# Kernel optimization log

Measured on AMD Instinct MI355X. Metric: run time of the kernel, lower is better.

Reference implementation:

```python
import jax, jax.numpy as jnp
import numpy as np


def _pairwise_sq_dist_mean(x):
    """Mean over feature dim of pairwise squared distances: D[i,j] = mean_k (x[j,k]-x[i,k])^2.
    Uses the ||a||^2 + ||b||^2 - 2ab identity instead of the O(n^2*d) broadcast."""
    d = x.shape[1]
    sq = jnp.sum(x * x, axis=1)  # [n]
    gram = x @ x.T               # [n, n]
    return (sq[:, None] + sq[None, :] - 2.0 * gram) / d


def setup_inputs() -> dict:
    key = jax.random.key(0)
    k1, k2 = jax.random.split(key)
    noises = jax.random.normal(k1, (4096, 256), dtype=jnp.float32)
    images = jax.random.normal(k2, (4096, 3, 64, 64), dtype=jnp.float32)
    return {"noises": noises, "images": images}


def reference(noises, images):
    if images.ndim > 2:
        images = images.reshape(images.shape[0], -1)
    images_dist = _pairwise_sq_dist_mean(images)  # [B, B]
    noises_dist = _pairwise_sq_dist_mean(noises)  # [B, B]
    return jnp.exp(jnp.mean(-images_dist * noises_dist))
```

## Files before the change

kernel.cpp:

```cpp
#include <hip/hip_runtime.h>
#include <stdint.h>
#include <math.h>

typedef __attribute__((ext_vector_type(8))) short short8;
typedef __attribute__((ext_vector_type(4))) float f32x4;

typedef __attribute__((address_space(1))) const uint32_t g_u32;
typedef __attribute__((address_space(3))) uint32_t l_u32;

static __device__ __forceinline__ uint16_t f2bf(float f) {
  union { float f; uint32_t u; } v; v.f = f;
  uint32_t r = (v.u + 0x7FFFu + ((v.u >> 16) & 1u)) >> 16;
  return (uint16_t)r;
}

static __device__ __forceinline__ float bf2f(uint16_t u) {
  union { uint32_t u; float f; } v; v.u = ((uint32_t)u) << 16;
  return v.f;
}

static __device__ __forceinline__ float waveReduceSum(float x) {
#pragma unroll
  for (int m = 32; m > 0; m >>= 1) x += __shfl_xor(x, m, 64);
  return x;
}

__global__ __launch_bounds__(256) void k_zero(float* __restrict__ p, int n4) {
  const int i = blockIdx.x * 256 + threadIdx.x;
  if (i < n4) reinterpret_cast<float4*>(p)[i] = float4{0.f, 0.f, 0.f, 0.f};
}

__global__ __launch_bounds__(256) void k_nt(const float* __restrict__ N,
                                            uint16_t* __restrict__ Nt,
                                            float* __restrict__ b,
                                            float* __restrict__ sn) {
  __shared__ __align__(16) uint16_t T[256 * 72];
  const int i0 = blockIdx.x * 64;
  const int tid = threadIdx.x;
  const int wave = tid >> 6, lane = tid & 63;
  float sq[16];
  float snacc0 = 0.f, snacc1 = 0.f, snacc2 = 0.f, snacc3 = 0.f;
#pragma unroll
  for (int it = 0; it < 16; ++it) {
    const int k = wave + it * 4;
    const int l4 = lane * 4;
    const float4 v = *reinterpret_cast<const float4*>(N + (size_t)(i0 + k) * 256 + l4);
    T[(l4 + 0) * 72 + k] = f2bf(v.x);
    T[(l4 + 1) * 72 + k] = f2bf(v.y);
    T[(l4 + 2) * 72 + k] = f2bf(v.z);
    T[(l4 + 3) * 72 + k] = f2bf(v.w);
    sq[it] = v.x * v.x + v.y * v.y + v.z * v.z + v.w * v.w;
    snacc0 += v.x; snacc1 += v.y; snacc2 += v.z; snacc3 += v.w;
  }
#pragma unroll
  for (int m = 1; m < 64; m <<= 1) {
#pragma unroll
    for (int it = 0; it < 16; ++it) sq[it] += __shfl_xor(sq[it], m, 64);
  }
  float myv = sq[0];
#pragma unroll
  for (int it = 1; it < 16; ++it) myv = (lane == it) ? sq[it] : myv;
  if (lane < 16) b[i0 + wave + lane * 4] = myv;
  {
    const int l4 = lane * 4;
    atomicAdd(&sn[l4 + 0], snacc0); atomicAdd(&sn[l4 + 1], snacc1);
    atomicAdd(&sn[l4 + 2], snacc2); atomicAdd(&sn[l4 + 3], snacc3);
  }
  __syncthreads();
  const int l = tid;
#pragma unroll
  for (int tt = 0; tt < 2; ++tt) {
    const int tg = blockIdx.x * 2 + tt;
#pragma unroll
    for (int c = 0; c < 4; ++c) {
      const short8 v = *reinterpret_cast<const short8*>(&T[l * 72 + tt * 32 + c * 8]);
      *reinterpret_cast<short8*>((char*)Nt + (size_t)tg * 16384 + l * 64 +
                                 ((c ^ (l & 3)) << 4)) = v;
    }
  }
}

__global__ __launch_bounds__(256) void k_h1(const float* __restrict__ N,
                                            const float* __restrict__ sn,
                                            float* __restrict__ h1) {
  const int wave = threadIdx.x >> 6, lane = threadIdx.x & 63;
  const int i = blockIdx.x * 4 + wave;
  const float4 v = *reinterpret_cast<const float4*>(N + (size_t)i * 256 + lane * 4);
  const float4 s = *reinterpret_cast<const float4*>(sn + lane * 4);
  float d = v.x * s.x + v.y * s.y + v.z * s.z + v.w * s.w;
  d = waveReduceSum(d);
  if (lane == 0) h1[i] = d;
}

__global__ __launch_bounds__(256, 3) void k_gemm_f3(const float* __restrict__ X,
                                                    const uint16_t* __restrict__ Nt,
                                                    uint16_t* __restrict__ Mb,
                                                    const float* __restrict__ bvec,
                                                    const float* __restrict__ h1v,
                                                    float* __restrict__ sx,
                                                    float* __restrict__ cx,
                                                    float* __restrict__ scal,
                                                    int B, int D1) {
  __shared__ __align__(16) uint16_t NB[2][8192];
  __shared__ __align__(16) uint16_t AB[2][64 * 40];
  __shared__ float SR[3][4];
  const int tid = threadIdx.x;
  const int w = tid >> 6, lane = tid & 63;
  const int lr = lane & 15, lh = lane >> 4;
  const int nks = B >> 7;
  const int pt = blockIdx.x >> 2, kc = blockIdx.x & 3;
  const int pbase = pt << 6;
  const int ks0 = kc * nks;

  f32x4 acc[4][4];
#pragma unroll
  for (int i = 0; i < 4; ++i)
#pragma unroll
    for (int j = 0; j < 4; ++j) acc[i][j] = (f32x4){0.f, 0.f, 0.f, 0.f};

  const int ap = tid & 63, ak8 = (tid >> 6) << 3;
  const float* Xbase = X + (size_t)(ks0 * 32 + ak8) * D1 + pbase + ap;
  float xr[8];
  float4 bv0, bv1, hv0, hv1;
  float s1 = 0.f, sb = 0.f, sh = 0.f, sxa = 0.f, cxa = 0.f;

#define GLL_B(S, BUF)                                                              \
  {                                                                                \
    const char* gsrc_ = (const char*)Nt + (size_t)(ks0 + (S)) * 16384 +            \
                        ((size_t)w << 10) + (size_t)lane * 16;                     \
    _Pragma("unroll")                                                              \
    for (int j_ = 0; j_ < 4; ++j_) {                                               \
      __builtin_amdgcn_global_load_lds((g_u32*)(gsrc_ + ((size_t)j_ << 12)),       \
                                       (l_u32*)&NB[BUF][(j_ * 4 + w) << 9],        \
                                       16, 0, 0);                                  \
    }                                                                              \
  }
#define A_LOADS(S)                                                                 \
  {                                                                                \
    const float* p_ = Xbase + (size_t)(S) * 32 * D1;                               \
    _Pragma("unroll")                                                              \
    for (int r_ = 0; r_ < 8; ++r_) xr[r_] = p_[(size_t)r_ * D1];                   \
    const int ib_ = ks0 * 32 + (S) * 32 + ak8;                                     \
    bv0 = *reinterpret_cast<const float4*>(bvec + ib_);                            \
    bv1 = *reinterpret_cast<const float4*>(bvec + ib_ + 4);                        \
    hv0 = *reinterpret_cast<const float4*>(h1v + ib_);                             \
    hv1 = *reinterpret_cast<const float4*>(h1v + ib_ + 4);                         \
  }

  GLL_B(0, 0);
  A_LOADS(0);

  for (int s = 0; s < nks; ++s) {
    const int buf = s & 1;
    {
      union { uint16_t u[8]; short8 v; } pk;
      const float bb[8] = {bv0.x, bv0.y, bv0.z, bv0.w, bv1.x, bv1.y, bv1.z, bv1.w};
      const float hh[8] = {hv0.x, hv0.y, hv0.z, hv0.w, hv1.x, hv1.y, hv1.z, hv1.w};
#pragma unroll
      for (int r = 0; r < 8; ++r) {
        const float x = xr[r];
        pk.u[r] = f2bf(x);
        const float x2 = x * x;
        s1 += x2;
        sb += bb[r] * x2;
        sh += hh[r] * x2;
        sxa += x;
        cxa += bb[r] * x;
      }
      *reinterpret_cast<short8*>(&AB[buf][ap * 40 + ak8]) = pk.v;
    }
    __syncthreads();
    if (s + 1 < nks) {
      GLL_B(s + 1, buf ^ 1);
      A_LOADS(s + 1);
    }
    short8 af[4], bfv[4];
#pragma unroll
    for (int ps = 0; ps < 4; ++ps)
      af[ps] = *reinterpret_cast<const short8*>(&AB[buf][(ps * 16 + lr) * 40 + lh * 8]);
#pragma unroll
    for (int q = 0; q < 4; ++q) {
      const int l = (w << 6) + (q << 4) + lr;
      bfv[q] = *reinterpret_cast<const short8*>(&NB[buf][l * 32 + ((lh ^ (l & 3)) << 3)]);
    }
#pragma unroll
    for (int ps = 0; ps < 4; ++ps)
#pragma unroll
      for (int q = 0; q < 4; ++q)
        acc[ps][q] = __builtin_amdgcn_mfma_f32_16x16x32_bf16(af[ps], bfv[q], acc[ps][q], 0, 0, 0);
    __syncthreads();
  }
#undef GLL_B
#undef A_LOADS

  uint16_t* Mk = Mb + (size_t)kc * ((size_t)D1 * 256);
#pragma unroll
  for (int ps = 0; ps < 4; ++ps)
#pragma unroll
    for (int q = 0; q < 4; ++q) {
      const int l = (w << 6) + (q << 4) + lr;
      const int p0 = pbase + ps * 16 + lh * 4;
      ushort4 st;
      st.x = f2bf(acc[ps][q][0]); st.y = f2bf(acc[ps][q][1]);
      st.z = f2bf(acc[ps][q][2]); st.w = f2bf(acc[ps][q][3]);
      *reinterpret_cast<ushort4*>(&Mk[(size_t)l * D1 + p0]) = st;
    }

  atomicAdd(&sx[pbase + ap], sxa);
  atomicAdd(&cx[pbase + ap], cxa);

  s1 = waveReduceSum(s1); sb = waveReduceSum(sb); sh = waveReduceSum(sh);
  if (lane == 0) { SR[0][w] = s1; SR[1][w] = sb; SR[2][w] = sh; }
  __syncthreads();
  if (tid == 0) {
    atomicAdd(&scal[0], SR[0][0] + SR[0][1] + SR[0][2] + SR[0][3]);
    atomicAdd(&scal[1], SR[1][0] + SR[1][1] + SR[1][2] + SR[1][3]);
    atomicAdd(&scal[2], SR[2][0] + SR[2][1] + SR[2][2] + SR[2][3]);
  }
}

__global__ __launch_bounds__(256) void k_square(const uint16_t* __restrict__ Mb,
                                                float* __restrict__ Fp,
                                                int n8, int slice) {
  __shared__ float red[4];
  float s = 0.f;
  for (int idx = blockIdx.x * 256 + threadIdx.x; idx < n8; idx += gridDim.x * 256) {
    union { short8 v; uint16_t u[8]; } m0, m1, m2, m3;
    m0.v = *reinterpret_cast<const short8*>(Mb + (size_t)idx * 8);
    m1.v = *reinterpret_cast<const short8*>(Mb + (size_t)idx * 8 + (size_t)slice);
    m2.v = *reinterpret_cast<const short8*>(Mb + (size_t)idx * 8 + 2 * (size_t)slice);
    m3.v = *reinterpret_cast<const short8*>(Mb + (size_t)idx * 8 + 3 * (size_t)slice);
#pragma unroll
    for (int e = 0; e < 8; ++e) {
      const float v = bf2f(m0.u[e]) + bf2f(m1.u[e]) + bf2f(m2.u[e]) + bf2f(m3.u[e]);
      s += v * v;
    }
  }
  s = waveReduceSum(s);
  const int wave = threadIdx.x >> 6, lane = threadIdx.x & 63;
  if (lane == 0) red[wave] = s;
  __syncthreads();
  if (threadIdx.x == 0) atomicAdd(Fp, red[0] + red[1] + red[2] + red[3]);
}

__global__ __launch_bounds__(256) void k_final3(const float* __restrict__ scal,
                                                const float* __restrict__ b,
                                                const float* __restrict__ sx,
                                                const float* __restrict__ cx,
                                                float* __restrict__ out,
                                                int B, int D1) {
  const int tid = threadIdx.x;
  float sb_ = 0.f, t2_ = 0.f;
  for (int i = tid; i < B; i += 256) sb_ += b[i];
  for (int k = tid; k < D1; k += 256) t2_ += sx[k] * cx[k];
  sb_ = waveReduceSum(sb_); t2_ = waveReduceSum(t2_);
  __shared__ float R[2][4];
  const int wave = tid >> 6, lane = tid & 63;
  if (lane == 0) { R[0][wave] = sb_; R[1][wave] = t2_; }
  __syncthreads();
  if (tid == 0) {
    double Sb = 0, T2 = 0;
    for (int w = 0; w < 4; ++w) { Sb += R[0][w]; T2 += R[1][w]; }
    const double Sa = scal[0], Sab = scal[1], T1 = scal[2], F = scal[3];
    const double total = 2.0 * (double)B * Sab + 2.0 * Sa * Sb - 4.0 * T1 - 4.0 * T2 + 4.0 * F;
    const double denom = (double)D1 * 256.0 * (double)B * (double)B;
    out[0] = (float)exp(-total / denom);
  }
}

__global__ __launch_bounds__(256) void k_noise_b(const float* __restrict__ N,
                                                 float* __restrict__ b) {
  const int wave = threadIdx.x >> 6, lane = threadIdx.x & 63;
  const int i = blockIdx.x * 4 + wave;
  const float4 v = *reinterpret_cast<const float4*>(N + (size_t)i * 256 + lane * 4);
  float s = v.x * v.x + v.y * v.y + v.z * v.z + v.w * v.w;
  s = waveReduceSum(s);
  if (lane == 0) b[i] = s;
}

__global__ __launch_bounds__(256) void k_x_pass(const float* __restrict__ X,
                                                const float* __restrict__ b,
                                                float* __restrict__ a,
                                                float* __restrict__ sx,
                                                float* __restrict__ cx, int D1) {
  const int ncb = D1 >> 10;
  const int colblk = blockIdx.x % ncb;
  const int rowblk = blockIdx.x / ncb;
  const int wv = threadIdx.x >> 6, lane = threadIdx.x & 63;
  const int col = (colblk << 10) + (wv << 8) + (lane << 2);
  const int row0 = rowblk << 6;
  float s0 = 0.f, s1 = 0.f, s2 = 0.f, s3 = 0.f;
  float c0 = 0.f, c1 = 0.f, c2 = 0.f, c3 = 0.f;
  const float* p = X + (size_t)row0 * D1 + col;
  for (int r8 = 0; r8 < 64; r8 += 8) {
    float asq[8];
#pragma unroll
    for (int r = 0; r < 8; ++r) {
      const float4 v = *reinterpret_cast<const float4*>(p + (size_t)(r8 + r) * D1);
      const float bi = b[row0 + r8 + r];
      s0 += v.x; s1 += v.y; s2 += v.z; s3 += v.w;
      c0 += bi * v.x; c1 += bi * v.y; c2 += bi * v.z; c3 += bi * v.w;
      asq[r] = v.x * v.x + v.y * v.y + v.z * v.z + v.w * v.w;
    }
#pragma unroll
    for (int m = 1; m < 64; m <<= 1) {
#pragma unroll
      for (int r = 0; r < 8; ++r) asq[r] += __shfl_xor(asq[r], m, 64);
    }
    float myv = asq[0];
#pragma unroll
    for (int r = 1; r < 8; ++r) myv = (lane == r) ? asq[r] : myv;
    if (lane < 8) atomicAdd(&a[row0 + r8 + lane], myv);
  }
  atomicAdd(&sx[col + 0], s0); atomicAdd(&sx[col + 1], s1);
  atomicAdd(&sx[col + 2], s2); atomicAdd(&sx[col + 3], s3);
  atomicAdd(&cx[col + 0], c0); atomicAdd(&cx[col + 1], c1);
  atomicAdd(&cx[col + 2], c2); atomicAdd(&cx[col + 3], c3);
}

__global__ __launch_bounds__(256) void k_noise2(const float* __restrict__ N,
                                                const float* __restrict__ a,
                                                float* __restrict__ sn,
                                                float* __restrict__ an) {
  const int t = threadIdx.x;
  const int i0 = blockIdx.x << 6;
  float ssn = 0.f, san = 0.f;
  for (int r = 0; r < 64; ++r) {
    const int i = i0 + r;
    const float v = N[(size_t)i * 256 + t];
    ssn += v;
    san += a[i] * v;
  }
  atomicAdd(&sn[t], ssn);
  atomicAdd(&an[t], san);
}

__global__ __launch_bounds__(256) void k_gemm_f(const float* __restrict__ X,
                                                const float* __restrict__ Nz,
                                                float* __restrict__ Fout,
                                                int B, int D1) {
  __shared__ uint16_t Abf[64 * 40];
  __shared__ uint16_t Bbf[256 * 40];
  __shared__ float red[4];
  const int tid = threadIdx.x;
  const int pbase = blockIdx.x << 6;
  const int wave = tid >> 6, lane = tid & 63;
  const int lr = lane & 15, lh = lane >> 4;

  f32x4 acc[4][4];
#pragma unroll
  for (int i = 0; i < 4; ++i)
#pragma unroll
    for (int j = 0; j < 4; ++j) acc[i][j] = (f32x4){0.f, 0.f, 0.f, 0.f};

  const int igx = tid & 7, p4x = ((tid >> 3) & 15) << 2;
  const int ign0 = tid & 7, l4n0 = (tid >> 3) << 2;
  const int ign1 = (tid + 256) & 7, l4n1 = ((tid + 256) >> 3) << 2;

  float4 xr0, xr1, xr2, xr3;
  float4 n0r0, n0r1, n0r2, n0r3;
  float4 n1r0, n1r1, n1r2, n1r3;

  auto load_stage = [&](int i0) {
    if (tid < 128) {
      const float* src = X + (size_t)(i0 + igx * 4) * D1 + pbase + p4x;
      xr0 = *reinterpret_cast<const float4*>(src);
      xr1 = *reinterpret_cast<const float4*>(src + D1);
      xr2 = *reinterpret_cast<const float4*>(src + 2 * (size_t)D1);
      xr3 = *reinterpret_cast<const float4*>(src + 3 * (size_t)D1);
    }
    {
      const float* src = Nz + (size_t)(i0 + ign0 * 4) * 256 + l4n0;
      n0r0 = *reinterpret_cast<const float4*>(src);
      n0r1 = *reinterpret_cast<const float4*>(src + 256);
      n0r2 = *reinterpret_cast<const float4*>(src + 512);
      n0r3 = *reinterpret_cast<const float4*>(src + 768);
    }
    {
      const float* src = Nz + (size_t)(i0 + ign1 * 4) * 256 + l4n1;
      n1r0 = *reinterpret_cast<const float4*>(src);
      n1r1 = *reinterpret_cast<const float4*>(src + 256);
      n1r2 = *reinterpret_cast<const float4*>(src + 512);
      n1r3 = *reinterpret_cast<const float4*>(src + 768);
    }
  };

  auto store_stage = [&]() {
    ushort4 w;
    if (tid < 128) {
      w.x = f2bf(xr0.x); w.y = f2bf(xr1.x); w.z = f2bf(xr2.x); w.w = f2bf(xr3.x);
      *reinterpret_cast<ushort4*>(&Abf[(p4x + 0) * 40 + igx * 4]) = w;
      w.x = f2bf(xr0.y); w.y = f2bf(xr1.y); w.z = f2bf(xr2.y); w.w = f2bf(xr3.y);
      *reinterpret_cast<ushort4*>(&Abf[(p4x + 1) * 40 + igx * 4]) = w;
      w.x = f2bf(xr0.z); w.y = f2bf(xr1.z); w.z = f2bf(xr2.z); w.w = f2bf(xr3.z);
      *reinterpret_cast<ushort4*>(&Abf[(p4x + 2) * 40 + igx * 4]) = w;
      w.x = f2bf(xr0.w); w.y = f2bf(xr1.w); w.z = f2bf(xr2.w); w.w = f2bf(xr3.w);
      *reinterpret_cast<ushort4*>(&Abf[(p4x + 3) * 40 + igx * 4]) = w;
    }
    w.x = f2bf(n0r0.x); w.y = f2bf(n0r1.x); w.z = f2bf(n0r2.x); w.w = f2bf(n0r3.x);
    *reinterpret_cast<ushort4*>(&Bbf[(l4n0 + 0) * 40 + ign0 * 4]) = w;
    w.x = f2bf(n0r0.y); w.y = f2bf(n0r1.y); w.z = f2bf(n0r2.y); w.w = f2bf(n0r3.y);
    *reinterpret_cast<ushort4*>(&Bbf[(l4n0 + 1) * 40 + ign0 * 4]) = w;
    w.x = f2bf(n0r0.z); w.y = f2bf(n0r1.z); w.z = f2bf(n0r2.z); w.w = f2bf(n0r3.z);
    *reinterpret_cast<ushort4*>(&Bbf[(l4n0 + 2) * 40 + ign0 * 4]) = w;
    w.x = f2bf(n0r0.w); w.y = f2bf(n0r1.w); w.z = f2bf(n0r2.w); w.w = f2bf(n0r3.w);
    *reinterpret_cast<ushort4*>(&Bbf[(l4n0 + 3) * 40 + ign0 * 4]) = w;

    w.x = f2bf(n1r0.x); w.y = f2bf(n1r1.x); w.z = f2bf(n1r2.x); w.w = f2bf(n1r3.x);
    *reinterpret_cast<ushort4*>(&Bbf[(l4n1 + 0) * 40 + ign1 * 4]) = w;
    w.x = f2bf(n1r0.y); w.y = f2bf(n1r1.y); w.z = f2bf(n1r2.y); w.w = f2bf(n1r3.y);
    *reinterpret_cast<ushort4*>(&Bbf[(l4n1 + 1) * 40 + ign1 * 4]) = w;
    w.x = f2bf(n1r0.z); w.y = f2bf(n1r1.z); w.z = f2bf(n1r2.z); w.w = f2bf(n1r3.z);
    *reinterpret_cast<ushort4*>(&Bbf[(l4n1 + 2) * 40 + ign1 * 4]) = w;
    w.x = f2bf(n1r0.w); w.y = f2bf(n1r1.w); w.z = f2bf(n1r2.w); w.w = f2bf(n1r3.w);
    *reinterpret_cast<ushort4*>(&Bbf[(l4n1 + 3) * 40 + ign1 * 4]) = w;
  };

  load_stage(0);
  for (int i0 = 0; i0 < B; i0 += 32) {
    store_stage();
    __syncthreads();
    if (i0 + 32 < B) load_stage(i0 + 32);

    short8 af[4], bfv[4];
#pragma unroll
    for (int ps = 0; ps < 4; ++ps)
      af[ps] = *reinterpret_cast<const short8*>(&Abf[(ps * 16 + lr) * 40 + lh * 8]);
#pragma unroll
    for (int q = 0; q < 4; ++q)
      bfv[q] = *reinterpret_cast<const short8*>(&Bbf[((wave * 4 + q) * 16 + lr) * 40 + lh * 8]);
#pragma unroll
    for (int ps = 0; ps < 4; ++ps)
#pragma unroll
      for (int q = 0; q < 4; ++q)
        acc[ps][q] = __builtin_amdgcn_mfma_f32_16x16x32_bf16(af[ps], bfv[q], acc[ps][q], 0, 0, 0);
    __syncthreads();
  }

  float loc = 0.f;
#pragma unroll
  for (int ps = 0; ps < 4; ++ps)
#pragma unroll
    for (int q = 0; q < 4; ++q)
#pragma unroll
      for (int e = 0; e < 4; ++e) loc += acc[ps][q][e] * acc[ps][q][e];
  loc = waveReduceSum(loc);
  if (lane == 0) red[wave] = loc;
  __syncthreads();
  if (tid == 0) atomicAdd(Fout, red[0] + red[1] + red[2] + red[3]);
}

__global__ __launch_bounds__(256) void k_final(const float* __restrict__ a,
                                               const float* __restrict__ b,
                                               const float* __restrict__ sx,
                                               const float* __restrict__ cx,
                                               const float* __restrict__ sn,
                                               const float* __restrict__ an,
                                               const float* __restrict__ Fp,
                                               float* __restrict__ out, int B, int D1) {
  const int tid = threadIdx.x;
  float sa = 0.f, sb = 0.f, sab = 0.f, t2 = 0.f;
  for (int i = tid; i < B; i += 256) {
    const float ai = a[i], bi = b[i];
    sa += ai; sb += bi; sab += ai * bi;
  }
  float t1 = an[tid] * sn[tid];
  for (int k = tid; k < D1; k += 256) t2 += cx[k] * sx[k];

  sa = waveReduceSum(sa); sb = waveReduceSum(sb); sab = waveReduceSum(sab);
  t1 = waveReduceSum(t1); t2 = waveReduceSum(t2);
  __shared__ float R[5][4];
  const int wave = tid >> 6, lane = tid & 63;
  if (lane == 0) { R[0][wave] = sa; R[1][wave] = sb; R[2][wave] = sab; R[3][wave] = t1; R[4][wave] = t2; }
  __syncthreads();
  if (tid == 0) {
    double Sa = 0, Sb = 0, Sab = 0, T1 = 0, T2 = 0;
    for (int w = 0; w < 4; ++w) {
      Sa += R[0][w]; Sb += R[1][w]; Sab += R[2][w]; T1 += R[3][w]; T2 += R[4][w];
    }
    const double F = (double)Fp[0];
    const double total = 2.0 * (double)B * Sab + 2.0 * Sa * Sb - 4.0 * T1 - 4.0 * T2 + 4.0 * F;
    const double denom = (double)D1 * 256.0 * (double)B * (double)B;
    out[0] = (float)exp(-total / denom);
  }
}

extern "C" void kernel_launch(void* const* d_in, const int* in_sizes, int n_in,
                              void* d_out, int out_size, void* d_ws, size_t ws_size,
                              hipStream_t stream) {
  const float* noises = (const float*)d_in[0];
  const float* images = (const float*)d_in[1];
  const int B = in_sizes[0] / 256;
  const int D1 = in_sizes[1] / B;
  float* outf = (float*)d_out;
  float* ws = (float*)d_ws;

  float* sx   = ws;
  float* cx   = ws + D1;
  float* sn   = ws + 2 * D1;
  float* scal = ws + 2 * D1 + 256;
  float* b    = ws + 2 * D1 + 272;
  float* h1   = b + B;
  const size_t nt_off_f = (size_t)2 * D1 + 272 + 2 * (size_t)B;
  const size_t nt_off_a = (nt_off_f + 3) & ~(size_t)3;
  uint16_t* Nt = (uint16_t*)(ws + nt_off_a);
  const size_t mb_off_f = nt_off_a + ((size_t)B * 256) / 2;
  uint16_t* Mb = (uint16_t*)(ws + mb_off_f);
  const size_t need = (mb_off_f + 2 * (size_t)D1 * 256) * sizeof(float);

  if (ws_size >= need) {
    const int nzero4 = (2 * D1 + 272) / 4;
    k_zero<<<(nzero4 + 255) / 256, 256, 0, stream>>>(ws, nzero4);
    k_nt<<<B / 64, 256, 0, stream>>>(noises, Nt, b, sn);
    k_h1<<<B / 4, 256, 0, stream>>>(noises, sn, h1);
    k_gemm_f3<<<(D1 / 64) * 4, 256, 0, stream>>>(images, Nt, Mb, b, h1, sx, cx, scal, B, D1);
    k_square<<<512, 256, 0, stream>>>(Mb, &scal[3], D1 * 256 / 8, D1 * 256);
    k_final3<<<1, 256, 0, stream>>>(scal, b, sx, cx, outf, B, D1);
  } else {
    float* a2  = ws;
    float* b2  = ws + B;
    float* sx2 = ws + 2 * B;
    float* cx2 = ws + 2 * B + D1;
    float* sn2 = ws + 2 * B + 2 * D1;
    float* an2 = ws + 2 * B + 2 * D1 + 256;
    float* Fp2 = ws + 2 * B + 2 * D1 + 512;
    const int nzero4 = (2 * B + 2 * D1 + 516) / 4;
    k_zero<<<(nzero4 + 255) / 256, 256, 0, stream>>>(ws, nzero4);
    k_noise_b<<<B / 4, 256, 0, stream>>>(noises, b2);
    k_x_pass<<<(D1 / 1024) * (B / 64), 256, 0, stream>>>(images, b2, a2, sx2, cx2, D1);
    k_noise2<<<B / 64, 256, 0, stream>>>(noises, a2, sn2, an2);
    k_gemm_f<<<D1 / 64, 256, 0, stream>>>(images, noises, Fp2, B, D1);
    k_final<<<1, 256, 0, stream>>>(a2, b2, sx2, cx2, sn2, an2, Fp2, outf, B, D1);
  }
}
```

Before: 151.5 us.

## Split image transpose/bf16 packing into separate pass feeding a pure-MFMA GEMM

```diff
diff --git a/kernel.cpp b/kernel.cpp
--- a/kernel.cpp
+++ b/kernel.cpp
@@ -90,6 +90,211 @@
   float d = v.x * s.x + v.y * s.y + v.z * s.z + v.w * s.w;
   d = waveReduceSum(d);
   if (lane == 0) h1[i] = d;
+}
+
+__global__ __launch_bounds__(256) void k_xt(const float* __restrict__ X,
+                                            const float* __restrict__ b,
+                                            const float* __restrict__ h1,
+                                            uint16_t* __restrict__ Xt,
+                                            float* __restrict__ sx,
+                                            float* __restrict__ cx,
+                                            float* __restrict__ scalA,
+                                            int B, int D1) {
+  __shared__ float T[64 * 65];
+  __shared__ float colS[64], colC[64];
+  __shared__ float SR[3][4];
+  const int tid = threadIdx.x;
+  const int npt = D1 >> 6;
+  const int pt = blockIdx.x % npt;
+  const int ti = blockIdx.x / npt;
+  const int i0 = ti << 6, p0 = pt << 6;
+  if (tid < 64) { colS[tid] = 0.f; colC[tid] = 0.f; }
+  __syncthreads();
+
+  const int r0 = tid >> 4;
+  const int c4 = (tid & 15) << 2;
+  float s1 = 0.f, sb = 0.f, sh = 0.f;
+  float cs0 = 0.f, cs1 = 0.f, cs2 = 0.f, cs3 = 0.f;
+  float cc0 = 0.f, cc1 = 0.f, cc2 = 0.f, cc3 = 0.f;
+#pragma unroll
+  for (int rr = 0; rr < 4; ++rr) {
+    const int r = r0 + rr * 16;
+    const int i = i0 + r;
+    const float4 v = *reinterpret_cast<const float4*>(X + (size_t)i * D1 + p0 + c4);
+    const float bi = b[i], hi = h1[i];
+    const float d = v.x * v.x + v.y * v.y + v.z * v.z + v.w * v.w;
+    s1 += d; sb += bi * d; sh += hi * d;
+    cs0 += v.x; cs1 += v.y; cs2 += v.z; cs3 += v.w;
+    cc0 += bi * v.x; cc1 += bi * v.y; cc2 += bi * v.z; cc3 += bi * v.w;
+    *reinterpret_cast<float4*>(&T[r * 65 + c4]) = v;
+  }
+  atomicAdd(&colS[c4 + 0], cs0); atomicAdd(&colS[c4 + 1], cs1);
+  atomicAdd(&colS[c4 + 2], cs2); atomicAdd(&colS[c4 + 3], cs3);
+  atomicAdd(&colC[c4 + 0], cc0); atomicAdd(&colC[c4 + 1], cc1);
+  atomicAdd(&colC[c4 + 2], cc2); atomicAdd(&colC[c4 + 3], cc3);
+  __syncthreads();
+
+  const int pl = tid >> 2;
+  const int slot = tid & 3;
+  const int oct = slot ^ (pl & 3);
+  uint16_t* img = Xt + ((size_t)pt * (B >> 5) + (size_t)(ti << 1)) * 2048;
+  {
+    union { uint16_t u[8]; short8 v8; } pk;
+#pragma unroll
+    for (int j = 0; j < 8; ++j) pk.u[j] = f2bf(T[(oct * 8 + j) * 65 + pl]);
+    *reinterpret_cast<short8*>(img + tid * 8) = pk.v8;
+#pragma unroll
+    for (int j = 0; j < 8; ++j) pk.u[j] = f2bf(T[(32 + oct * 8 + j) * 65 + pl]);
+    *reinterpret_cast<short8*>(img + 2048 + tid * 8) = pk.v8;
+  }
+
+  s1 = waveReduceSum(s1); sb = waveReduceSum(sb); sh = waveReduceSum(sh);
+  const int wave = tid >> 6, lane = tid & 63;
+  if (lane == 0) { SR[0][wave] = s1; SR[1][wave] = sb; SR[2][wave] = sh; }
+  if (tid < 64) {
+    atomicAdd(&sx[p0 + tid], colS[tid]);
+    atomicAdd(&cx[p0 + tid], colC[tid]);
+  }
+  __syncthreads();
+  if (tid == 0) {
+    float* slotp = scalA + (size_t)(blockIdx.x & 63) * 4;
+    atomicAdd(&slotp[0], SR[0][0] + SR[0][1] + SR[0][2] + SR[0][3]);
+    atomicAdd(&slotp[1], SR[1][0] + SR[1][1] + SR[1][2] + SR[1][3]);
+    atomicAdd(&slotp[2], SR[2][0] + SR[2][1] + SR[2][2] + SR[2][3]);
+  }
+}
+
+__global__ __launch_bounds__(256, 3) void k_gemm_f4(const uint16_t* __restrict__ Xt,
+                                                    const uint16_t* __restrict__ Nt,
+                                                    uint16_t* __restrict__ Mb,
+                                                    int B, int D1) {
+  __shared__ __align__(16) uint16_t NB[2][8192];
+  __shared__ __align__(16) uint16_t AB[2][2048];
+  const int tid = threadIdx.x;
+  const int w = tid >> 6, lane = tid & 63;
+  const int lr = lane & 15, lh = lane >> 4;
+  const int nks = B >> 7;
+  const int tks = B >> 5;
+  const int pt = blockIdx.x >> 2, kc = blockIdx.x & 3;
+  const int pbase = pt << 6;
+  const int ks0 = kc * nks;
+
+  f32x4 acc[4][4];
+#pragma unroll
+  for (int i = 0; i < 4; ++i)
+#pragma unroll
+    for (int j = 0; j < 4; ++j) acc[i][j] = (f32x4){0.f, 0.f, 0.f, 0.f};
+
+#define GLL_AB(S, BUF)                                                             \
+  {                                                                                \
+    const char* bs_ = (const char*)Nt + (size_t)(ks0 + (S)) * 16384 +              \
+                      ((size_t)w << 10) + (size_t)lane * 16;                       \
+    _Pragma("unroll")                                                              \
+    for (int j_ = 0; j_ < 4; ++j_) {                                               \
+      __builtin_amdgcn_global_load_lds((g_u32*)(bs_ + ((size_t)j_ << 12)),         \
+                                       (l_u32*)&NB[BUF][(j_ * 4 + w) << 9],        \
+                                       16, 0, 0);                                  \
+    }                                                                              \
+    const char* as_ = (const char*)Xt + ((size_t)pt * tks + ks0 + (S)) * 4096 +    \
+                      ((size_t)w << 10) + (size_t)lane * 16;                       \
+    __builtin_amdgcn_global_load_lds((g_u32*)as_, (l_u32*)&AB[BUF][w << 9],        \
+                                     16, 0, 0);                                    \
+  }
+
+  GLL_AB(0, 0);
+  for (int s = 0; s < nks; ++s) {
+    const int buf = s & 1;
+    __syncthreads();
+    if (s + 1 < nks) GLL_AB(s + 1, buf ^ 1);
+    short8 af[4], bfv[4];
+#pragma unroll
+    for (int ps = 0; ps < 4; ++ps) {
+      const int p = ps * 16 + lr;
+      af[ps] = *reinterpret_cast<const short8*>(&AB[buf][p * 32 + ((lh ^ (p & 3)) << 3)]);
+    }
+#pragma unroll
+    for (int q = 0; q < 4; ++q) {
+      const int l = (w << 6) + (q << 4) + lr;
+      bfv[q] = *reinterpret_cast<const short8*>(&NB[buf][l * 32 + ((lh ^ (l & 3)) << 3)]);
+    }
+#pragma unroll
+    for (int ps = 0; ps < 4; ++ps)
+#pragma unroll
+      for (int q = 0; q < 4; ++q)
+        acc[ps][q] = __builtin_amdgcn_mfma_f32_16x16x32_bf16(af[ps], bfv[q], acc[ps][q], 0, 0, 0);
+  }
+#undef GLL_AB
+
+  uint16_t* Mk = Mb + (size_t)kc * ((size_t)D1 * 256);
+#pragma unroll
+  for (int ps = 0; ps < 4; ++ps)
+#pragma unroll
+    for (int q = 0; q < 4; ++q) {
+      const int l = (w << 6) + (q << 4) + lr;
+      const int p0e = pbase + ps * 16 + lh * 4;
+      ushort4 st;
+      st.x = f2bf(acc[ps][q][0]); st.y = f2bf(acc[ps][q][1]);
+      st.z = f2bf(acc[ps][q][2]); st.w = f2bf(acc[ps][q][3]);
+      *reinterpret_cast<ushort4*>(&Mk[(size_t)l * D1 + p0e]) = st;
+    }
+}
+
+__global__ __launch_bounds__(256) void k_square(const uint16_t* __restrict__ Mb,
+                                                float* __restrict__ Fp,
+                                                int n8, int slice) {
+  __shared__ float red[4];
+  float s = 0.f;
+  for (int idx = blockIdx.x * 256 + threadIdx.x; idx < n8; idx += gridDim.x * 256) {
+    union { short8 v; uint16_t u[8]; } m0, m1, m2, m3;
+    m0.v = *reinterpret_cast<const short8*>(Mb + (size_t)idx * 8);
+    m1.v = *reinterpret_cast<const short8*>(Mb + (size_t)idx * 8 + (size_t)slice);
+    m2.v = *reinterpret_cast<const short8*>(Mb + (size_t)idx * 8 + 2 * (size_t)slice);
+    m3.v = *reinterpret_cast<const short8*>(Mb + (size_t)idx * 8 + 3 * (size_t)slice);
+#pragma unroll
+    for (int e = 0; e < 8; ++e) {
+      const float v = bf2f(m0.u[e]) + bf2f(m1.u[e]) + bf2f(m2.u[e]) + bf2f(m3.u[e]);
+      s += v * v;
+    }
+  }
+  s = waveReduceSum(s);
+  const int wave = threadIdx.x >> 6, lane = threadIdx.x & 63;
+  if (lane == 0) red[wave] = s;
+  __syncthreads();
+  if (threadIdx.x == 0) atomicAdd(Fp, red[0] + red[1] + red[2] + red[3]);
+}
+
+__global__ __launch_bounds__(256) void k_final4(const float* __restrict__ scalA,
+                                                const float* __restrict__ Fp,
+                                                const float* __restrict__ b,
+                                                const float* __restrict__ sx,
+                                                const float* __restrict__ cx,
+                                                float* __restrict__ out,
+                                                int B, int D1) {
+  const int tid = threadIdx.x;
+  float sa_ = 0.f, sab_ = 0.f, t1_ = 0.f, sb_ = 0.f, t2_ = 0.f;
+  if (tid < 64) {
+    sa_ = scalA[tid * 4 + 0];
+    sab_ = scalA[tid * 4 + 1];
+    t1_ = scalA[tid * 4 + 2];
+  }
+  for (int i = tid; i < B; i += 256) sb_ += b[i];
+  for (int k = tid; k < D1; k += 256) t2_ += sx[k] * cx[k];
+  sa_ = waveReduceSum(sa_); sab_ = waveReduceSum(sab_); t1_ = waveReduceSum(t1_);
+  sb_ = waveReduceSum(sb_); t2_ = waveReduceSum(t2_);
+  __shared__ float R[5][4];
+  const int wave = tid >> 6, lane = tid & 63;
+  if (lane == 0) { R[0][wave] = sa_; R[1][wave] = sab_; R[2][wave] = t1_; R[3][wave] = sb_; R[4][wave] = t2_; }
+  __syncthreads();
+  if (tid == 0) {
+    double Sa = 0, Sab = 0, T1 = 0, Sb = 0, T2 = 0;
+    for (int w = 0; w < 4; ++w) {
+      Sa += R[0][w]; Sab += R[1][w]; T1 += R[2][w]; Sb += R[3][w]; T2 += R[4][w];
+    }
+    const double F = (double)Fp[0];
+    const double total = 2.0 * (double)B * Sab + 2.0 * Sa * Sb - 4.0 * T1 - 4.0 * T2 + 4.0 * F;
+    const double denom = (double)D1 * 256.0 * (double)B * (double)B;
+    out[0] = (float)exp(-total / denom);
+  }
 }
 
 __global__ __launch_bounds__(256, 3) void k_gemm_f3(const float* __restrict__ X,
@@ -161,11 +366,8 @@
         const float x = xr[r];
         pk.u[r] = f2bf(x);
         const float x2 = x * x;
-        s1 += x2;
-        sb += bb[r] * x2;
-        sh += hh[r] * x2;
-        sxa += x;
-        cxa += bb[r] * x;
+        s1 += x2; sb += bb[r] * x2; sh += hh[r] * x2;
+        sxa += x; cxa += bb[r] * x;
       }
       *reinterpret_cast<short8*>(&AB[buf][ap * 40 + ak8]) = pk.v;
     }
@@ -217,30 +419,6 @@
     atomicAdd(&scal[1], SR[1][0] + SR[1][1] + SR[1][2] + SR[1][3]);
     atomicAdd(&scal[2], SR[2][0] + SR[2][1] + SR[2][2] + SR[2][3]);
   }
-}
-
-__global__ __launch_bounds__(256) void k_square(const uint16_t* __restrict__ Mb,
-                                                float* __restrict__ Fp,
-                                                int n8, int slice) {
-  __shared__ float red[4];
-  float s = 0.f;
-  for (int idx = blockIdx.x * 256 + threadIdx.x; idx < n8; idx += gridDim.x * 256) {
-    union { short8 v; uint16_t u[8]; } m0, m1, m2, m3;
-    m0.v = *reinterpret_cast<const short8*>(Mb + (size_t)idx * 8);
-    m1.v = *reinterpret_cast<const short8*>(Mb + (size_t)idx * 8 + (size_t)slice);
-    m2.v = *reinterpret_cast<const short8*>(Mb + (size_t)idx * 8 + 2 * (size_t)slice);
-    m3.v = *reinterpret_cast<const short8*>(Mb + (size_t)idx * 8 + 3 * (size_t)slice);
-#pragma unroll
-    for (int e = 0; e < 8; ++e) {
-      const float v = bf2f(m0.u[e]) + bf2f(m1.u[e]) + bf2f(m2.u[e]) + bf2f(m3.u[e]);
-      s += v * v;
-    }
-  }
-  s = waveReduceSum(s);
-  const int wave = threadIdx.x >> 6, lane = threadIdx.x & 63;
-  if (lane == 0) red[wave] = s;
-  __syncthreads();
-  if (threadIdx.x == 0) atomicAdd(Fp, red[0] + red[1] + red[2] + red[3]);
 }
 
 __global__ __launch_bounds__(256) void k_final3(const float* __restrict__ scal,
@@ -268,223 +446,6 @@
   }
 }
 
-__global__ __launch_bounds__(256) void k_noise_b(const float* __restrict__ N,
-                                                 float* __restrict__ b) {
-  const int wave = threadIdx.x >> 6, lane = threadIdx.x & 63;
-  const int i = blockIdx.x * 4 + wave;
-  const float4 v = *reinterpret_cast<const float4*>(N + (size_t)i * 256 + lane * 4);
-  float s = v.x * v.x + v.y * v.y + v.z * v.z + v.w * v.w;
-  s = waveReduceSum(s);
-  if (lane == 0) b[i] = s;
-}
-
-__global__ __launch_bounds__(256) void k_x_pass(const float* __restrict__ X,
-                                                const float* __restrict__ b,
-                                                float* __restrict__ a,
-                                                float* __restrict__ sx,
-                                                float* __restrict__ cx, int D1) {
-  const int ncb = D1 >> 10;
-  const int colblk = blockIdx.x % ncb;
-  const int rowblk = blockIdx.x / ncb;
-  const int wv = threadIdx.x >> 6, lane = threadIdx.x & 63;
-  const int col = (colblk << 10) + (wv << 8) + (lane << 2);
-  const int row0 = rowblk << 6;
-  float s0 = 0.f, s1 = 0.f, s2 = 0.f, s3 = 0.f;
-  float c0 = 0.f, c1 = 0.f, c2 = 0.f, c3 = 0.f;
-  const float* p = X + (size_t)row0 * D1 + col;
-  for (int r8 = 0; r8 < 64; r8 += 8) {
-    float asq[8];
-#pragma unroll
-    for (int r = 0; r < 8; ++r) {
-      const float4 v = *reinterpret_cast<const float4*>(p + (size_t)(r8 + r) * D1);
-      const float bi = b[row0 + r8 + r];
-      s0 += v.x; s1 += v.y; s2 += v.z; s3 += v.w;
-      c0 += bi * v.x; c1 += bi * v.y; c2 += bi * v.z; c3 += bi * v.w;
-      asq[r] = v.x * v.x + v.y * v.y + v.z * v.z + v.w * v.w;
-    }
-#pragma unroll
-    for (int m = 1; m < 64; m <<= 1) {
-#pragma unroll
-      for (int r = 0; r < 8; ++r) asq[r] += __shfl_xor(asq[r], m, 64);
-    }
-    float myv = asq[0];
-#pragma unroll
-    for (int r = 1; r < 8; ++r) myv = (lane == r) ? asq[r] : myv;
-    if (lane < 8) atomicAdd(&a[row0 + r8 + lane], myv);
-  }
-  atomicAdd(&sx[col + 0], s0); atomicAdd(&sx[col + 1], s1);
-  atomicAdd(&sx[col + 2], s2); atomicAdd(&sx[col + 3], s3);
-  atomicAdd(&cx[col + 0], c0); atomicAdd(&cx[col + 1], c1);
-  atomicAdd(&cx[col + 2], c2); atomicAdd(&cx[col + 3], c3);
-}
-
-__global__ __launch_bounds__(256) void k_noise2(const float* __restrict__ N,
-                                                const float* __restrict__ a,
-                                                float* __restrict__ sn,
-                                                float* __restrict__ an) {
-  const int t = threadIdx.x;
-  const int i0 = blockIdx.x << 6;
-  float ssn = 0.f, san = 0.f;
-  for (int r = 0; r < 64; ++r) {
-    const int i = i0 + r;
-    const float v = N[(size_t)i * 256 + t];
-    ssn += v;
-    san += a[i] * v;
-  }
-  atomicAdd(&sn[t], ssn);
-  atomicAdd(&an[t], san);
-}
-
-__global__ __launch_bounds__(256) void k_gemm_f(const float* __restrict__ X,
-                                                const float* __restrict__ Nz,
-                                                float* __restrict__ Fout,
-                                                int B, int D1) {
-  __shared__ uint16_t Abf[64 * 40];
-  __shared__ uint16_t Bbf[256 * 40];
-  __shared__ float red[4];
-  const int tid = threadIdx.x;
-  const int pbase = blockIdx.x << 6;
-  const int wave = tid >> 6, lane = tid & 63;
-  const int lr = lane & 15, lh = lane >> 4;
-
-  f32x4 acc[4][4];
-#pragma unroll
-  for (int i = 0; i < 4; ++i)
-#pragma unroll
-    for (int j = 0; j < 4; ++j) acc[i][j] = (f32x4){0.f, 0.f, 0.f, 0.f};
-
-  const int igx = tid & 7, p4x = ((tid >> 3) & 15) << 2;
-  const int ign0 = tid & 7, l4n0 = (tid >> 3) << 2;
-  const int ign1 = (tid + 256) & 7, l4n1 = ((tid + 256) >> 3) << 2;
-
-  float4 xr0, xr1, xr2, xr3;
-  float4 n0r0, n0r1, n0r2, n0r3;
-  float4 n1r0, n1r1, n1r2, n1r3;
-
-  auto load_stage = [&](int i0) {
-    if (tid < 128) {
-      const float* src = X + (size_t)(i0 + igx * 4) * D1 + pbase + p4x;
-      xr0 = *reinterpret_cast<const float4*>(src);
-      xr1 = *reinterpret_cast<const float4*>(src + D1);
-      xr2 = *reinterpret_cast<const float4*>(src + 2 * (size_t)D1);
-      xr3 = *reinterpret_cast<const float4*>(src + 3 * (size_t)D1);
-    }
-    {
-      const float* src = Nz + (size_t)(i0 + ign0 * 4) * 256 + l4n0;
-      n0r0 = *reinterpret_cast<const float4*>(src);
-      n0r1 = *reinterpret_cast<const float4*>(src + 256);
-      n0r2 = *reinterpret_cast<const float4*>(src + 512);
-      n0r3 = *reinterpret_cast<const float4*>(src + 768);
-    }
-    {
-      const float* src = Nz + (size_t)(i0 + ign1 * 4) * 256 + l4n1;
-      n1r0 = *reinterpret_cast<const float4*>(src);
-      n1r1 = *reinterpret_cast<const float4*>(src + 256);
-      n1r2 = *reinterpret_cast<const float4*>(src + 512);
-      n1r3 = *reinterpret_cast<const float4*>(src + 768);
-    }
-  };
-
-  auto store_stage = [&]() {
-    ushort4 w;
-    if (tid < 128) {
-      w.x = f2bf(xr0.x); w.y = f2bf(xr1.x); w.z = f2bf(xr2.x); w.w = f2bf(xr3.x);
-      *reinterpret_cast<ushort4*>(&Abf[(p4x + 0) * 40 + igx * 4]) = w;
-      w.x = f2bf(xr0.y); w.y = f2bf(xr1.y); w.z = f2bf(xr2.y); w.w = f2bf(xr3.y);
-      *reinterpret_cast<ushort4*>(&Abf[(p4x + 1) * 40 + igx * 4]) = w;
-      w.x = f2bf(xr0.z); w.y = f2bf(xr1.z); w.z = f2bf(xr2.z); w.w = f2bf(xr3.z);
-      *reinterpret_cast<ushort4*>(&Abf[(p4x + 2) * 40 + igx * 4]) = w;
-      w.x = f2bf(xr0.w); w.y = f2bf(xr1.w); w.z = f2bf(xr2.w); w.w = f2bf(xr3.w);
-      *reinterpret_cast<ushort4*>(&Abf[(p4x + 3) * 40 + igx * 4]) = w;
-    }
-    w.x = f2bf(n0r0.x); w.y = f2bf(n0r1.x); w.z = f2bf(n0r2.x); w.w = f2bf(n0r3.x);
-    *reinterpret_cast<ushort4*>(&Bbf[(l4n0 + 0) * 40 + ign0 * 4]) = w;
-    w.x = f2bf(n0r0.y); w.y = f2bf(n0r1.y); w.z = f2bf(n0r2.y); w.w = f2bf(n0r3.y);
-    *reinterpret_cast<ushort4*>(&Bbf[(l4n0 + 1) * 40 + ign0 * 4]) = w;
-    w.x = f2bf(n0r0.z); w.y = f2bf(n0r1.z); w.z = f2bf(n0r2.z); w.w = f2bf(n0r3.z);
-    *reinterpret_cast<ushort4*>(&Bbf[(l4n0 + 2) * 40 + ign0 * 4]) = w;
-    w.x = f2bf(n0r0.w); w.y = f2bf(n0r1.w); w.z = f2bf(n0r2.w); w.w = f2bf(n0r3.w);
-    *reinterpret_cast<ushort4*>(&Bbf[(l4n0 + 3) * 40 + ign0 * 4]) = w;
-
-    w.x = f2bf(n1r0.x); w.y = f2bf(n1r1.x); w.z = f2bf(n1r2.x); w.w = f2bf(n1r3.x);
-    *reinterpret_cast<ushort4*>(&Bbf[(l4n1 + 0) * 40 + ign1 * 4]) = w;
-    w.x = f2bf(n1r0.y); w.y = f2bf(n1r1.y); w.z = f2bf(n1r2.y); w.w = f2bf(n1r3.y);
-    *reinterpret_cast<ushort4*>(&Bbf[(l4n1 + 1) * 40 + ign1 * 4]) = w;
-    w.x = f2bf(n1r0.z); w.y = f2bf(n1r1.z); w.z = f2bf(n1r2.z); w.w = f2bf(n1r3.z);
-    *reinterpret_cast<ushort4*>(&Bbf[(l4n1 + 2) * 40 + ign1 * 4]) = w;
-    w.x = f2bf(n1r0.w); w.y = f2bf(n1r1.w); w.z = f2bf(n1r2.w); w.w = f2bf(n1r3.w);
-    *reinterpret_cast<ushort4*>(&Bbf[(l4n1 + 3) * 40 + ign1 * 4]) = w;
-  };
-
-  load_stage(0);
-  for (int i0 = 0; i0 < B; i0 += 32) {
-    store_stage();
-    __syncthreads();
-    if (i0 + 32 < B) load_stage(i0 + 32);
-
-    short8 af[4], bfv[4];
-#pragma unroll
-    for (int ps = 0; ps < 4; ++ps)
-      af[ps] = *reinterpret_cast<const short8*>(&Abf[(ps * 16 + lr) * 40 + lh * 8]);
-#pragma unroll
-    for (int q = 0; q < 4; ++q)
-      bfv[q] = *reinterpret_cast<const short8*>(&Bbf[((wave * 4 + q) * 16 + lr) * 40 + lh * 8]);
-#pragma unroll
-    for (int ps = 0; ps < 4; ++ps)
-#pragma unroll
-      for (int q = 0; q < 4; ++q)
-        acc[ps][q] = __builtin_amdgcn_mfma_f32_16x16x32_bf16(af[ps], bfv[q], acc[ps][q], 0, 0, 0);
-    __syncthreads();
-  }
-
-  float loc = 0.f;
-#pragma unroll
-  for (int ps = 0; ps < 4; ++ps)
-#pragma unroll
-    for (int q = 0; q < 4; ++q)
-#pragma unroll
-      for (int e = 0; e < 4; ++e) loc += acc[ps][q][e] * acc[ps][q][e];
-  loc = waveReduceSum(loc);
-  if (lane == 0) red[wave] = loc;
-  __syncthreads();
-  if (tid == 0) atomicAdd(Fout, red[0] + red[1] + red[2] + red[3]);
-}
-
-__global__ __launch_bounds__(256) void k_final(const float* __restrict__ a,
-                                               const float* __restrict__ b,
-                                               const float* __restrict__ sx,
-                                               const float* __restrict__ cx,
-                                               const float* __restrict__ sn,
-                                               const float* __restrict__ an,
-                                               const float* __restrict__ Fp,
-                                               float* __restrict__ out, int B, int D1) {
-  const int tid = threadIdx.x;
-  float sa = 0.f, sb = 0.f, sab = 0.f, t2 = 0.f;
-  for (int i = tid; i < B; i += 256) {
-    const float ai = a[i], bi = b[i];
-    sa += ai; sb += bi; sab += ai * bi;
-  }
-  float t1 = an[tid] * sn[tid];
-  for (int k = tid; k < D1; k += 256) t2 += cx[k] * sx[k];
-
-  sa = waveReduceSum(sa); sb = waveReduceSum(sb); sab = waveReduceSum(sab);
-  t1 = waveReduceSum(t1); t2 = waveReduceSum(t2);
-  __shared__ float R[5][4];
-  const int wave = tid >> 6, lane = tid & 63;
-  if (lane == 0) { R[0][wave] = sa; R[1][wave] = sb; R[2][wave] = sab; R[3][wave] = t1; R[4][wave] = t2; }
-  __syncthreads();
-  if (tid == 0) {
-    double Sa = 0, Sb = 0, Sab = 0, T1 = 0, T2 = 0;
-    for (int w = 0; w < 4; ++w) {
-      Sa += R[0][w]; Sb += R[1][w]; Sab += R[2][w]; T1 += R[3][w]; T2 += R[4][w];
-    }
-    const double F = (double)Fp[0];
-    const double total = 2.0 * (double)B * Sab + 2.0 * Sa * Sb - 4.0 * T1 - 4.0 * T2 + 4.0 * F;
-    const double denom = (double)D1 * 256.0 * (double)B * (double)B;
-    out[0] = (float)exp(-total / denom);
-  }
-}
-
 extern "C" void kernel_launch(void* const* d_in, const int* in_sizes, int n_in,
                               void* d_out, int out_size, void* d_ws, size_t ws_size,
                               hipStream_t stream) {
@@ -495,41 +456,48 @@
   float* outf = (float*)d_out;
   float* ws = (float*)d_ws;
 
-  float* sx   = ws;
-  float* cx   = ws + D1;
-  float* sn   = ws + 2 * D1;
-  float* scal = ws + 2 * D1 + 256;
-  float* b    = ws + 2 * D1 + 272;
-  float* h1   = b + B;
-  const size_t nt_off_f = (size_t)2 * D1 + 272 + 2 * (size_t)B;
-  const size_t nt_off_a = (nt_off_f + 3) & ~(size_t)3;
-  uint16_t* Nt = (uint16_t*)(ws + nt_off_a);
-  const size_t mb_off_f = nt_off_a + ((size_t)B * 256) / 2;
-  uint16_t* Mb = (uint16_t*)(ws + mb_off_f);
-  const size_t need = (mb_off_f + 2 * (size_t)D1 * 256) * sizeof(float);
-
-  if (ws_size >= need) {
-    const int nzero4 = (2 * D1 + 272) / 4;
+  float* sx    = ws;
+  float* cx    = ws + D1;
+  float* sn    = ws + 2 * D1;
+  float* scalA = ws + 2 * D1 + 256;
+  float* Fp    = ws + 2 * D1 + 512;
+  float* b     = ws + 2 * D1 + 544;
+  float* h1    = b + B;
+  const size_t nt_off = ((size_t)2 * D1 + 544 + 2 * (size_t)B + 3) & ~(size_t)3;
+  uint16_t* Nt = (uint16_t*)(ws + nt_off);
+  const size_t xt_off = nt_off + ((size_t)B * 256) / 2;
+  uint16_t* Xt = (uint16_t*)(ws + xt_off);
+  const size_t xt_floats = ((size_t)D1 / 64) * ((size_t)B / 32) * 1024;
+  const size_t mb_off = xt_off + xt_floats;
+  uint16_t* Mb = (uint16_t*)(ws + mb_off);
+  const size_t need1 = (mb_off + 2 * (size_t)D1 * 256) * sizeof(float);
+
+  if (ws_size >= need1) {
+    const int nzero4 = (2 * D1 + 544) / 4;
     k_zero<<<(nzero4 + 255) / 256, 256, 0, stream>>>(ws, nzero4);
     k_nt<<<B / 64, 256, 0, stream>>>(noises, Nt, b, sn);
     k_h1<<<B / 4, 256, 0, stream>>>(noises, sn, h1);
-    k_gemm_f3<<<(D1 / 64) * 4, 256, 0, stream>>>(images, Nt, Mb, b, h1, sx, cx, scal, B, D1);
-    k_square<<<512, 256, 0, stream>>>(Mb, &scal[3], D1 * 256 / 8, D1 * 256);
-    k_final3<<<1, 256, 0, stream>>>(scal, b, sx, cx, outf, B, D1);
+    k_xt<<<(B / 64) * (D1 / 64), 256, 0, stream>>>(images, b, h1, Xt, sx, cx, scalA, B, D1);
+    k_gemm_f4<<<(D1 / 64) * 4, 256, 0, stream>>>(Xt, Nt, Mb, B, D1);
+    k_square<<<512, 256, 0, stream>>>(Mb, Fp, D1 * 256 / 8, D1 * 256);
+    k_final4<<<1, 256, 0, stream>>>(scalA, Fp, b, sx, cx, outf, B, D1);
   } else {
-    float* a2  = ws;
-    float* b2  = ws + B;
-    float* sx2 = ws + 2 * B;
-    float* cx2 = ws + 2 * B + D1;
-    float* sn2 = ws + 2 * B + 2 * D1;
-    float* an2 = ws + 2 * B + 2 * D1 + 256;
-    float* Fp2 = ws + 2 * B + 2 * D1 + 512;
-    const int nzero4 = (2 * B + 2 * D1 + 516) / 4;
+    float* sx2   = ws;
+    float* cx2   = ws + D1;
+    float* sn2   = ws + 2 * D1;
+    float* scal2 = ws + 2 * D1 + 256;
+    float* b2    = ws + 2 * D1 + 272;
+    float* h12   = b2 + B;
+    const size_t nt2_off = ((size_t)2 * D1 + 272 + 2 * (size_t)B + 3) & ~(size_t)3;
+    uint16_t* Nt2 = (uint16_t*)(ws + nt2_off);
+    const size_t mb2_off = nt2_off + ((size_t)B * 256) / 2;
+    uint16_t* Mb2 = (uint16_t*)(ws + mb2_off);
+    const int nzero4 = (2 * D1 + 272) / 4;
     k_zero<<<(nzero4 + 255) / 256, 256, 0, stream>>>(ws, nzero4);
-    k_noise_b<<<B / 4, 256, 0, stream>>>(noises, b2);
-    k_x_pass<<<(D1 / 1024) * (B / 64), 256, 0, stream>>>(images, b2, a2, sx2, cx2, D1);
-    k_noise2<<<B / 64, 256, 0, stream>>>(noises, a2, sn2, an2);
-    k_gemm_f<<<D1 / 64, 256, 0, stream>>>(images, noises, Fp2, B, D1);
-    k_final<<<1, 256, 0, stream>>>(a2, b2, sx2, cx2, sn2, an2, Fp2, outf, B, D1);
-  }
-}
+    k_nt<<<B / 64, 256, 0, stream>>>(noises, Nt2, b2, sn2);
+    k_h1<<<B / 4, 256, 0, stream>>>(noises, sn2, h12);
+    k_gemm_f3<<<(D1 / 64) * 4, 256, 0, stream>>>(images, Nt2, Mb2, b2, h12, sx2, cx2, scal2, B, D1);
+    k_square<<<512, 256, 0, stream>>>(Mb2, &scal2[3], D1 * 256 / 8, D1 * 256);
+    k_final3<<<1, 256, 0, stream>>>(scal2, b2, sx2, cx2, outf, B, D1);
+  }
+}
```

Result: slower. 254.6 us (+68.0%).
